# Kernel optimization log

Measured on AMD Instinct MI355X. Metric: run time of the kernel, lower is better.

The kernel has to match this reference:

```python
import jax, jax.numpy as jnp
import numpy as np

D_MODEL = 1024
D_HIDDEN = 4096
NUM_EXPERT = 8
TOP_K = 2
B, N = 1, 8192


def setup_inputs() -> dict:
    key = jax.random.key(0)
    ks = jax.random.split(key, 8)
    s1 = 1.0 / np.sqrt(D_MODEL)
    s2 = 1.0 / np.sqrt(D_HIDDEN)
    return {
        "x": jax.random.normal(ks[0], (B, N, D_MODEL), jnp.float32),
        "expert_tokens": jax.random.normal(ks[1], (NUM_EXPERT, D_MODEL), jnp.float32),
        "W1": jax.random.normal(ks[2], (NUM_EXPERT, D_MODEL, D_HIDDEN), jnp.float32) * s1,
        "b1": jnp.zeros((NUM_EXPERT, D_HIDDEN), jnp.float32),
        "W2": jax.random.normal(ks[3], (NUM_EXPERT, D_HIDDEN, D_HIDDEN), jnp.float32) * s2,
        "b2": jnp.zeros((NUM_EXPERT, D_HIDDEN), jnp.float32),
        "W3": jax.random.normal(ks[4], (NUM_EXPERT, D_HIDDEN, D_MODEL), jnp.float32) * s2,
        "b3": jnp.zeros((NUM_EXPERT, D_MODEL), jnp.float32),
    }


def _expert_mlp(x, W1, b1, W2, b2, W3, b3):
    # Linear -> GELU (exact, matching torch nn.GELU) -> Linear -> GELU -> Linear
    h = jax.nn.gelu(jnp.einsum("bnd,dh->bnh", x, W1) + b1, approximate=False)
    h = jax.nn.gelu(jnp.einsum("bnh,hk->bnk", h, W2) + b2, approximate=False)
    return jnp.einsum("bnh,hd->bnd", h, W3) + b3


def reference(x, expert_tokens, W1, b1, W2, b2, W3, b3):
    # router scores: [B, N, E]
    scores = jnp.einsum("bnd,ed->bne", x, expert_tokens)
    _, topk_idx = jax.lax.top_k(scores, TOP_K)  # [B, N, TOP_K]
    outputs = jnp.zeros_like(x)
    num_expert = W1.shape[0]
    for i in range(num_expert):
        # gate weight = (# of top-k slots assigned to expert i) / top_k
        w = jnp.mean((topk_idx == i).astype(x.dtype), axis=-1, keepdims=True)
        y = _expert_mlp(x, W1[i], b1[i], W2[i], b2[i], W3[i], b3[i])
        outputs = outputs + y * w
    return outputs
```

## Files before the change

### kernel.cpp

```cpp
#include <hip/hip_runtime.h>
#include <stdint.h>

#define D_MODEL 1024
#define D_HID   4096
#define NEXP    8
#define NTOK    8192
#define TOTROW  (NTOK*2)

typedef unsigned short ushort_t;
typedef __attribute__((ext_vector_type(8))) short short8;
typedef __attribute__((ext_vector_type(4))) float f32x4;

static __device__ __forceinline__ ushort_t f2bf(float f) {
    union { float f; uint32_t u; } v; v.f = f;
    uint32_t u = v.u;
    uint32_t r = (u + 0x7FFFu + ((u >> 16) & 1u)) >> 16;
    return (ushort_t)r;
}
static __device__ __forceinline__ float bf2f(ushort_t h) {
    union { uint32_t u; float f; } v; v.u = ((uint32_t)h) << 16;
    return v.f;
}
static __device__ __forceinline__ float gelu_f(float x) {
    return 0.5f * x * (1.0f + erff(x * 0.70710678118654752f));
}

static __device__ __forceinline__ void gload_lds16(const void* g, void* l) {
    __builtin_amdgcn_global_load_lds(
        (const __attribute__((address_space(1))) void*)g,
        (__attribute__((address_space(3))) void*)l,
        16, 0, 0);
}

__global__ __launch_bounds__(256) void router_kernel(
    const float* __restrict__ x, const float* __restrict__ et,
    int* __restrict__ cnt, int* __restrict__ top2)
{
    __shared__ float lds_et[NEXP * D_MODEL];
    int t = threadIdx.x;
    #pragma unroll
    for (int i = 0; i < (NEXP * D_MODEL) / 256; ++i)
        lds_et[i * 256 + t] = et[i * 256 + t];
    __syncthreads();

    int lane = t & 63, wv = t >> 6;
    int n = blockIdx.x * 4 + wv;
    double s[NEXP];
    #pragma unroll
    for (int e = 0; e < NEXP; ++e) s[e] = 0.0;
    const float* xr = x + (size_t)n * D_MODEL;
    for (int it = 0; it < D_MODEL / 64; ++it) {
        float xv = xr[it * 64 + lane];
        #pragma unroll
        for (int e = 0; e < NEXP; ++e)
            s[e] += (double)(xv * lds_et[e * D_MODEL + it * 64 + lane]);
    }
    #pragma unroll
    for (int e = 0; e < NEXP; ++e)
        for (int off = 32; off; off >>= 1)
            s[e] += __shfl_xor(s[e], off);

    if (lane == 0) {
        int e1 = 0;
        for (int e = 1; e < NEXP; ++e) if (s[e] > s[e1]) e1 = e;
        int e2 = (e1 == 0) ? 1 : 0;
        for (int e = 0; e < NEXP; ++e) if (e != e1 && s[e] > s[e2]) e2 = e;
        top2[n * 2 + 0] = e1;
        top2[n * 2 + 1] = e2;
        atomicAdd(&cnt[e1], 1);
        atomicAdd(&cnt[e2], 1);
    }
}

__global__ void scan_kernel(const int* __restrict__ cnt, int* __restrict__ base,
                            int* __restrict__ cnt2)
{
    if (threadIdx.x == 0 && blockIdx.x == 0) {
        int acc = 0;
        for (int e = 0; e < NEXP; ++e) { base[e] = acc; acc += cnt[e]; cnt2[e] = 0; }
    }
}

__global__ __launch_bounds__(256) void assign_kernel(
    const int* __restrict__ top2, const int* __restrict__ base,
    int* __restrict__ cnt2, int* __restrict__ rowinfo, int* __restrict__ token_rows)
{
    int n = blockIdx.x * 256 + threadIdx.x;
    if (n >= NTOK) return;
    #pragma unroll
    for (int k = 0; k < 2; ++k) {
        int e = top2[n * 2 + k];
        int slot = atomicAdd(&cnt2[e], 1);
        int row = base[e] + slot;
        rowinfo[row] = n;
        token_rows[n * 2 + k] = row;
    }
}

__global__ __launch_bounds__(256) void convert_x(
    const float* __restrict__ x, ushort_t* __restrict__ xb)
{
    size_t i = ((size_t)blockIdx.x * 256 + threadIdx.x) * 4;
    float4 f = *(const float4*)(x + i);
    ushort_t o[4];
    o[0] = f2bf(f.x); o[1] = f2bf(f.y); o[2] = f2bf(f.z); o[3] = f2bf(f.w);
    *(uint2*)(xb + i) = *(const uint2*)o;
}

__global__ __launch_bounds__(256) void transpose_kernel(
    const float* __restrict__ in, ushort_t* __restrict__ out, int K, int N)
{
    __shared__ float tile[64][65];
    int e = blockIdx.z;
    int k0 = blockIdx.y * 64, n0 = blockIdx.x * 64;
    const float* ine = in + (size_t)e * K * N + (size_t)k0 * N + n0;
    ushort_t* oute = out + (size_t)e * N * K + (size_t)n0 * K + k0;
    int t = threadIdx.x;
    int lr = t >> 4;
    int lc = (t & 15) * 4;
    #pragma unroll
    for (int i = 0; i < 4; ++i) {
        float4 v = *(const float4*)(ine + (size_t)(i * 16 + lr) * N + lc);
        tile[i * 16 + lr][lc + 0] = v.x;
        tile[i * 16 + lr][lc + 1] = v.y;
        tile[i * 16 + lr][lc + 2] = v.z;
        tile[i * 16 + lr][lc + 3] = v.w;
    }
    __syncthreads();
    int nr = t >> 3;
    int kg = (t & 7) * 8;
    #pragma unroll
    for (int j = 0; j < 2; ++j) {
        int n = j * 32 + nr;
        ushort_t o[8];
        #pragma unroll
        for (int m = 0; m < 8; ++m) o[m] = f2bf(tile[kg + m][n]);
        *(uint4*)(oute + (size_t)n * K + kg) = *(const uint4*)o;
    }
}


#define RD_A(BUF, MH) do {                                                        \
    _Pragma("unroll") for (int mi = 0; mi < 4; ++mi) {                            \
        areg[mi][0] = *(const short8*)(pA0 + (BUF)*16384 + (MH)*4096 + mi*1024);  \
        areg[mi][1] = *(const short8*)(pA1 + (BUF)*16384 + (MH)*4096 + mi*1024);  \
    }                                                                             \
} while (0)

#define RD_B(DST, BUF, NH) do {                                                   \
    _Pragma("unroll") for (int ni = 0; ni < 2; ++ni) {                            \
        DST[ni][0] = *(const short8*)(pB0 + (BUF)*16384 + (NH)*2048 + ni*1024);   \
        DST[ni][1] = *(const short8*)(pB1 + (BUF)*16384 + (NH)*2048 + ni*1024);   \
    }                                                                             \
} while (0)

#define PHASE(BUF, MH, NH, LA, LB, BREG, STAGE_STMT, TAIL_STMT)                   \
  do {                                                                            \
    if (LA) RD_A(BUF, MH);                                                        \
    if (LB) RD_B(BREG, BUF, NH);                                                  \
    STAGE_STMT;                                                                   \
    __builtin_amdgcn_s_barrier();                                                 \
    asm volatile("s_waitcnt lgkmcnt(0)" ::: "memory");                            \
    __builtin_amdgcn_s_setprio(1);                                                \
    _Pragma("unroll") for (int mi = 0; mi < 4; ++mi)                              \
    _Pragma("unroll") for (int ni = 0; ni < 2; ++ni)                              \
    _Pragma("unroll") for (int ks = 0; ks < 2; ++ks)                              \
      acc[(MH)*4 + mi][(NH)*2 + ni] = __builtin_amdgcn_mfma_f32_16x16x32_bf16(    \
          areg[mi][ks], BREG[ni][ks], acc[(MH)*4 + mi][(NH)*2 + ni], 0, 0, 0);    \
    __builtin_amdgcn_s_setprio(0);                                                \
    TAIL_STMT;                                                                    \
    __builtin_amdgcn_s_barrier();                                                 \
  } while (0)

#define VW4 asm volatile("s_waitcnt vmcnt(4)" ::: "memory")
#define VW0 asm volatile("s_waitcnt vmcnt(0)" ::: "memory")
#define VNO ((void)0)

template<bool GATHER, bool GELU_ACT>
__global__ __launch_bounds__(512, 2) void moe_gemm8(
    const ushort_t* __restrict__ Ah,
    const ushort_t* __restrict__ BT,
    const float* __restrict__ bias,
    ushort_t* __restrict__ C,
    const int* __restrict__ cnt, const int* __restrict__ basep,
    const int* __restrict__ rowinfo,
    int Ncols, int K)
{
    const int e = blockIdx.z;
    const int cnte = cnt[e];
    const int mt = blockIdx.y;
    if (mt * 256 >= cnte) return;
    const int base_e = basep[e];
    const int row0 = base_e + mt * 256;
    const int col0 = blockIdx.x * 256;

    __shared__ __attribute__((aligned(16))) ushort_t SMEM[2][2][256][64];

    const int t = threadIdx.x;
    const int lane = t & 63;
    const int wv = t >> 6;
    const int wm = wv >> 2;
    const int wn = wv & 3;
    const int l15 = lane & 15, lhi = lane >> 4;
    const int key = l15 & 7;
    const int lr8 = lane >> 3;
    const int sl  = (lane & 7) ^ lr8;

    const int slot0 = (lhi ^ key) * 8;
    const int slot1 = ((4 + lhi) ^ key) * 8;
    const ushort_t* pA0 = &SMEM[0][0][wm * 128 + l15][slot0];
    const ushort_t* pA1 = &SMEM[0][0][wm * 128 + l15][slot1];
    const ushort_t* pB0 = &SMEM[1][0][wn * 64 + l15][slot0];
    const ushort_t* pB1 = &SMEM[1][0][wn * 64 + l15][slot1];

    uint32_t aOff[2][2], bOff[2][2];
    #pragma unroll
    for (int mh = 0; mh < 2; ++mh)
        #pragma unroll
        for (int c = 0; c < 2; ++c) {
            int tr = mh * 64 + wv * 8 + lr8 + c * 128;
            int gr = row0 + tr; if (gr > TOTROW - 1) gr = TOTROW - 1;
            uint32_t rowid = GATHER ? (uint32_t)rowinfo[gr] : (uint32_t)gr;
            aOff[mh][c] = rowid * (uint32_t)(K * 2) + sl * 16;
        }
    #pragma unroll
    for (int nh = 0; nh < 2; ++nh)
        #pragma unroll
        for (int c = 0; c < 2; ++c) {
            int tr = (wv >> 2) * 64 + nh * 32 + (wv & 3) * 8 + lr8 + c * 128;
            bOff[nh][c] = ((uint32_t)e * Ncols + col0 + tr) * (uint32_t)(K * 2) + sl * 16;
        }

    const int arb = wv * 8;
    const int brb = (wv >> 2) * 64 + (wv & 3) * 8;

    auto stageA = [&](int buf, int mh) {
        gload_lds16((const char*)Ah + aOff[mh][0], (void*)&SMEM[0][buf][mh * 64 + arb][0]);
        gload_lds16((const char*)Ah + aOff[mh][1], (void*)&SMEM[0][buf][128 + mh * 64 + arb][0]);
        aOff[mh][0] += 128; aOff[mh][1] += 128;
    };
    auto stageB = [&](int buf, int nh) {
        gload_lds16((const char*)BT + bOff[nh][0], (void*)&SMEM[1][buf][nh * 32 + brb][0]);
        gload_lds16((const char*)BT + bOff[nh][1], (void*)&SMEM[1][buf][128 + nh * 32 + brb][0]);
        bOff[nh][0] += 128; bOff[nh][1] += 128;
    };

    f32x4 acc[8][4];
    #pragma unroll
    for (int i = 0; i < 8; ++i)
        #pragma unroll
        for (int j = 0; j < 4; ++j)
            acc[i][j] = (f32x4){0.f, 0.f, 0.f, 0.f};

    short8 areg[4][2], breg0[2][2], breg1[2][2];

    const int KT = K / 64;
    const int NIT = KT / 2;

    stageA(0, 0); stageA(0, 1); stageB(0, 0); stageB(0, 1);
    stageA(1, 0); stageB(1, 1);
    VW4;
    __builtin_amdgcn_s_barrier();

    for (int i2 = 0; i2 < NIT - 1; ++i2) {
         PHASE(0, 0, 0, true,  true,  breg0, stageA(1, 1), VNO);
         PHASE(0, 0, 1, false, true,  breg1, stageB(1, 0), VNO);
         PHASE(0, 1, 1, true,  false, breg1, stageA(0, 0), VNO);
         PHASE(0, 1, 0, false, false, breg0, stageB(0, 1), VW4);
         PHASE(1, 0, 0, true,  true,  breg0, stageA(0, 1), VNO);
         PHASE(1, 0, 1, false, true,  breg1, stageB(0, 0), VNO);
         PHASE(1, 1, 1, true,  false, breg1, stageA(1, 0), VNO);
         PHASE(1, 1, 0, false, false, breg0, stageB(1, 1), VW4);
    }
    {
         PHASE(0, 0, 0, true,  true,  breg0, stageA(1, 1), VNO);
         PHASE(0, 0, 1, false, true,  breg1, stageB(1, 0), VNO);
         PHASE(0, 1, 1, true,  false, breg1, VNO,          VNO);
         PHASE(0, 1, 0, false, false, breg0, VNO,          VW0);
         PHASE(1, 0, 0, true,  true,  breg0, VNO,          VNO);
         PHASE(1, 0, 1, false, true,  breg1, VNO,          VNO);
         PHASE(1, 1, 1, true,  false, breg1, VNO,          VNO);
        asm volatile("s_waitcnt lgkmcnt(0)" ::: "memory");
        #pragma unroll
        for (int mi = 0; mi < 4; ++mi)
            #pragma unroll
            for (int ni = 0; ni < 2; ++ni)
                #pragma unroll
                for (int ks = 0; ks < 2; ++ks)
                    acc[4 + mi][ni] = __builtin_amdgcn_mfma_f32_16x16x32_bf16(
                        areg[mi][ks], breg0[ni][ks], acc[4 + mi][ni], 0, 0, 0);
    }

    ushort_t* ctile = &SMEM[0][0][0][0];
    #pragma unroll
    for (int n = 0; n < 4; ++n) {
        int c = wn * 64 + n * 16 + l15;
        float bv = bias[e * Ncols + col0 + c];
        #pragma unroll
        for (int m = 0; m < 8; ++m) {
            #pragma unroll
            for (int q = 0; q < 4; ++q) {
                int r = wm * 128 + m * 16 + lhi * 4 + q;
                float v = acc[m][n][q] + bv;
                if (GELU_ACT) v = gelu_f(v);
                ctile[r * 256 + ((c >> 3) ^ ((r & 7) << 2)) * 8 + (c & 7)] = f2bf(v);
            }
        }
    }
    __syncthreads();
    {
        int rr = t >> 2;
        int ch0 = t & 3;
        #pragma unroll
        for (int pass = 0; pass < 2; ++pass) {
            int r = pass * 128 + rr;
            int rl = mt * 256 + r;
            if (rl < cnte) {
                size_t gbase = (size_t)(base_e + rl) * Ncols + col0;
                #pragma unroll
                for (int i = 0; i < 8; ++i) {
                    int ch = ch0 + i * 4;
                    uint4 v = *(const uint4*)&ctile[r * 256 + ((ch ^ ((r & 7) << 2)) * 8)];
                    *(uint4*)&C[gbase + ch * 8] = v;
                }
            }
        }
    }
}

__global__ __launch_bounds__(256) void combine_kernel(
    const ushort_t* __restrict__ Y, const int* __restrict__ token_rows,
    float* __restrict__ out)
{
    int n = blockIdx.x;
    int t = threadIdx.x;
    int r1 = token_rows[n * 2 + 0], r2 = token_rows[n * 2 + 1];
    const ushort_t* y1 = Y + (size_t)r1 * D_MODEL + t * 4;
    const ushort_t* y2 = Y + (size_t)r2 * D_MODEL + t * 4;
    ushort_t a[4], b[4];
    *(uint2*)a = *(const uint2*)y1;
    *(uint2*)b = *(const uint2*)y2;
    float4 o;
    o.x = 0.5f * (bf2f(a[0]) + bf2f(b[0]));
    o.y = 0.5f * (bf2f(a[1]) + bf2f(b[1]));
    o.z = 0.5f * (bf2f(a[2]) + bf2f(b[2]));
    o.w = 0.5f * (bf2f(a[3]) + bf2f(b[3]));
    *(float4*)(out + (size_t)n * D_MODEL + t * 4) = o;
}

extern "C" void kernel_launch(void* const* d_in, const int* in_sizes, int n_in,
                              void* d_out, int out_size, void* d_ws, size_t ws_size,
                              hipStream_t stream)
{
    const float* x  = (const float*)d_in[0];
    const float* et = (const float*)d_in[1];
    const float* W1 = (const float*)d_in[2];
    const float* b1 = (const float*)d_in[3];
    const float* W2 = (const float*)d_in[4];
    const float* b2 = (const float*)d_in[5];
    const float* W3 = (const float*)d_in[6];
    const float* b3 = (const float*)d_in[7];
    float* out = (float*)d_out;

    char* ws = (char*)d_ws;
    size_t off = 0;
    auto alloc = [&](size_t bytes) -> char* {
        char* p = ws + off;
        off += (bytes + 255) & ~(size_t)255;
        return p;
    };
    int* cnt        = (int*)alloc(NEXP * 4);
    int* basep      = (int*)alloc(NEXP * 4);
    int* cnt2       = (int*)alloc(NEXP * 4);
    int* top2       = (int*)alloc((size_t)NTOK * 2 * 4);
    int* token_rows = (int*)alloc((size_t)NTOK * 2 * 4);
    int* rowinfo    = (int*)alloc((size_t)TOTROW * 4);
    ushort_t* W1T = (ushort_t*)alloc((size_t)NEXP * D_HID * D_MODEL * 2);
    ushort_t* W2T = (ushort_t*)alloc((size_t)NEXP * D_HID * D_HID * 2);
    ushort_t* W3T = (ushort_t*)alloc((size_t)NEXP * D_MODEL * D_HID * 2);
    ushort_t* H1  = (ushort_t*)alloc((size_t)TOTROW * D_HID * 2);
    ushort_t* H2  = (ushort_t*)alloc((size_t)TOTROW * D_HID * 2);
    ushort_t* Yr  = (ushort_t*)alloc((size_t)TOTROW * D_MODEL * 2);
    if (off > ws_size) return;

    ushort_t* xb = H2;

    hipMemsetAsync(cnt, 0, NEXP * 4, stream);
    router_kernel<<<NTOK / 4, 256, 0, stream>>>(x, et, cnt, top2);
    scan_kernel<<<1, 64, 0, stream>>>(cnt, basep, cnt2);
    assign_kernel<<<NTOK / 256, 256, 0, stream>>>(top2, basep, cnt2, rowinfo, token_rows);

    convert_x<<<(NTOK * D_MODEL) / 1024, 256, 0, stream>>>(x, xb);

    transpose_kernel<<<dim3(D_HID / 64, D_MODEL / 64, NEXP), 256, 0, stream>>>(W1, W1T, D_MODEL, D_HID);
    transpose_kernel<<<dim3(D_HID / 64, D_HID / 64, NEXP), 256, 0, stream>>>(W2, W2T, D_HID, D_HID);
    transpose_kernel<<<dim3(D_MODEL / 64, D_HID / 64, NEXP), 256, 0, stream>>>(W3, W3T, D_HID, D_MODEL);

    moe_gemm8<true, true><<<dim3(D_HID / 256, 16, NEXP), 512, 0, stream>>>(
        xb, W1T, b1, H1, cnt, basep, rowinfo, D_HID, D_MODEL);
    moe_gemm8<false, true><<<dim3(D_HID / 256, 16, NEXP), 512, 0, stream>>>(
        H1, W2T, b2, H2, cnt, basep, rowinfo, D_HID, D_HID);
    moe_gemm8<false, false><<<dim3(D_MODEL / 256, 16, NEXP), 512, 0, stream>>>(
        H2, W3T, b3, Yr, cnt, basep, rowinfo, D_MODEL, D_HID);

    combine_kernel<<<NTOK, 256, 0, stream>>>(Yr, token_rows, out);
}
```

Baseline: 1.589 ms.

## Reschedule GEMM main loop to prefetch LDS fragments during MFMA phases

Restructures the 8-phase main loop of the expert GEMM so each phase issues MFMAs first, then in its tail stages the next global-to-LDS loads and reads the next phase's A/B register fragments from LDS. This removes the per-phase leading barrier and lgkmcnt wait before compute, so LDS reads overlap with the previous MFMA block. The prologue now fills both buffers fully and waits on all loads, and the vmcnt threshold changes to 6. The risk is an LDS read-after-write hazard if the single barrier per phase does not cover the buffer reuse, and more register pressure from the fragments kept live across phases.

```diff
diff --git a/kernel.cpp b/kernel.cpp
--- a/kernel.cpp
+++ b/kernel.cpp
@@ -154,27 +154,20 @@
     }                                                                             \
 } while (0)
 
-#define PHASE(BUF, MH, NH, LA, LB, BREG, STAGE_STMT, TAIL_STMT)                   \
-  do {                                                                            \
-    if (LA) RD_A(BUF, MH);                                                        \
-    if (LB) RD_B(BREG, BUF, NH);                                                  \
-    STAGE_STMT;                                                                   \
-    __builtin_amdgcn_s_barrier();                                                 \
-    asm volatile("s_waitcnt lgkmcnt(0)" ::: "memory");                            \
+#define MM(BR, MH, NH) do {                                                       \
     __builtin_amdgcn_s_setprio(1);                                                \
     _Pragma("unroll") for (int mi = 0; mi < 4; ++mi)                              \
     _Pragma("unroll") for (int ni = 0; ni < 2; ++ni)                              \
     _Pragma("unroll") for (int ks = 0; ks < 2; ++ks)                              \
       acc[(MH)*4 + mi][(NH)*2 + ni] = __builtin_amdgcn_mfma_f32_16x16x32_bf16(    \
-          areg[mi][ks], BREG[ni][ks], acc[(MH)*4 + mi][(NH)*2 + ni], 0, 0, 0);    \
+          areg[mi][ks], BR[ni][ks], acc[(MH)*4 + mi][(NH)*2 + ni], 0, 0, 0);      \
     __builtin_amdgcn_s_setprio(0);                                                \
-    TAIL_STMT;                                                                    \
-    __builtin_amdgcn_s_barrier();                                                 \
-  } while (0)
-
-#define VW4 asm volatile("s_waitcnt vmcnt(4)" ::: "memory")
+} while (0)
+
+#define PH(MH, NH, BR, TAIL) do { MM(BR, MH, NH); TAIL; __builtin_amdgcn_s_barrier(); } while (0)
+
+#define VW6 asm volatile("s_waitcnt vmcnt(6)" ::: "memory")
 #define VW0 asm volatile("s_waitcnt vmcnt(0)" ::: "memory")
-#define VNO ((void)0)
 
 template<bool GATHER, bool GELU_ACT>
 __global__ __launch_bounds__(512, 2) void moe_gemm8(
@@ -257,38 +250,31 @@
     const int KT = K / 64;
     const int NIT = KT / 2;
 
-    stageA(0, 0); stageA(0, 1); stageB(0, 0); stageB(0, 1);
-    stageA(1, 0); stageB(1, 1);
-    VW4;
+    stageA(0, 0); stageB(0, 0); stageB(0, 1); stageA(0, 1);
+    stageA(1, 0); stageB(1, 0); stageB(1, 1); stageA(1, 1);
+    VW0;
     __builtin_amdgcn_s_barrier();
+    RD_A(0, 0); RD_B(breg0, 0, 0);
 
     for (int i2 = 0; i2 < NIT - 1; ++i2) {
-         PHASE(0, 0, 0, true,  true,  breg0, stageA(1, 1), VNO);
-         PHASE(0, 0, 1, false, true,  breg1, stageB(1, 0), VNO);
-         PHASE(0, 1, 1, true,  false, breg1, stageA(0, 0), VNO);
-         PHASE(0, 1, 0, false, false, breg0, stageB(0, 1), VW4);
-         PHASE(1, 0, 0, true,  true,  breg0, stageA(0, 1), VNO);
-         PHASE(1, 0, 1, false, true,  breg1, stageB(0, 0), VNO);
-         PHASE(1, 1, 1, true,  false, breg1, stageA(1, 0), VNO);
-         PHASE(1, 1, 0, false, false, breg0, stageB(1, 1), VW4);
+         PH(0, 0, breg0, { stageA(0, 0); RD_B(breg1, 0, 1); });
+         PH(0, 1, breg1, { stageB(0, 0); RD_A(0, 1); });
+         PH(1, 1, breg1, { stageB(0, 1); VW6; });
+         PH(1, 0, breg0, { stageA(0, 1); RD_A(1, 0); RD_B(breg0, 1, 0); });
+         PH(0, 0, breg0, { stageA(1, 0); RD_B(breg1, 1, 1); });
+         PH(0, 1, breg1, { stageB(1, 0); RD_A(1, 1); });
+         PH(1, 1, breg1, { stageB(1, 1); VW6; });
+         PH(1, 0, breg0, { stageA(1, 1); RD_A(0, 0); RD_B(breg0, 0, 0); });
     }
     {
-         PHASE(0, 0, 0, true,  true,  breg0, stageA(1, 1), VNO);
-         PHASE(0, 0, 1, false, true,  breg1, stageB(1, 0), VNO);
-         PHASE(0, 1, 1, true,  false, breg1, VNO,          VNO);
-         PHASE(0, 1, 0, false, false, breg0, VNO,          VW0);
-         PHASE(1, 0, 0, true,  true,  breg0, VNO,          VNO);
-         PHASE(1, 0, 1, false, true,  breg1, VNO,          VNO);
-         PHASE(1, 1, 1, true,  false, breg1, VNO,          VNO);
-        asm volatile("s_waitcnt lgkmcnt(0)" ::: "memory");
-        #pragma unroll
-        for (int mi = 0; mi < 4; ++mi)
-            #pragma unroll
-            for (int ni = 0; ni < 2; ++ni)
-                #pragma unroll
-                for (int ks = 0; ks < 2; ++ks)
-                    acc[4 + mi][ni] = __builtin_amdgcn_mfma_f32_16x16x32_bf16(
-                        areg[mi][ks], breg0[ni][ks], acc[4 + mi][ni], 0, 0, 0);
+         PH(0, 0, breg0, { RD_B(breg1, 0, 1); });
+         PH(0, 1, breg1, { RD_A(0, 1); });
+         PH(1, 1, breg1, { VW0; });
+         PH(1, 0, breg0, { RD_A(1, 0); RD_B(breg0, 1, 0); });
+         PH(0, 0, breg0, { RD_B(breg1, 1, 1); });
+         PH(0, 1, breg1, { RD_A(1, 1); });
+         PH(1, 1, breg1, { });
+         MM(breg0, 1, 0);
     }
 
     ushort_t* ctile = &SMEM[0][0][0][0];
```

Result: faster. 1.502 ms (median of 2 runs) (-5.5%).
